# Kernel tuning notes

Hardware: AMD Instinct MI355X
Metric: run time of the kernel (lower is better)

## Reference

```python
import jax, jax.numpy as jnp
import numpy as np
from jax import lax

B, C, H, W = 32, 684, 28, 112   # batch, annotation channels, feature map HxW
Q, NP, N, K, PAD = 256, 512, 256, 11, 5  # f_channel, hidden_dim, decoder_dim, conv kernel, padding


def setup_inputs() -> dict:
    key = jax.random.key(0)
    ks = jax.random.split(key, 7)
    i = jax.random.normal(ks[0], (B, C, H, W), dtype=jnp.float32)
    hat_s_t = jax.random.normal(ks[1], (B, N), dtype=jnp.float32)
    alpha = jnp.zeros((B, 1, H, W), dtype=jnp.float32)  # coverage state (reset_alpha)
    conv_w = jax.random.normal(ks[2], (Q, 1, K, K), dtype=jnp.float32) * 0.02
    conv_b = jnp.zeros((Q,), dtype=jnp.float32)
    Wa = jax.random.normal(ks[3], (C, NP), dtype=jnp.float32) * (1.0 / np.sqrt(C))
    Wf = jax.random.normal(ks[4], (Q, NP), dtype=jnp.float32) * (1.0 / np.sqrt(Q))
    Ws = jax.random.normal(ks[5], (N, NP), dtype=jnp.float32) * (1.0 / np.sqrt(N))
    v = jax.random.normal(ks[6], (NP,), dtype=jnp.float32) * (1.0 / np.sqrt(NP))
    return {"i": i, "hat_s_t": hat_s_t, "alpha": alpha,
            "conv_w": conv_w, "conv_b": conv_b,
            "Wa": Wa, "Wf": Wf, "Ws": Ws, "v": v}


def reference(i, hat_s_t, alpha, conv_w, conv_b, Wa, Wf, Ws, v):
    b, c, h, w = i.shape
    L = h * w
    # coverage features: F = conv(alpha) -> [B, Q, H, W] -> [B, L, Q]
    F = lax.conv_general_dilated(
        alpha, conv_w, window_strides=(1, 1),
        padding=[(PAD, PAD), (PAD, PAD)],
        dimension_numbers=("NCHW", "OIHW", "NCHW"))
    F = F + conv_b[None, :, None, None]
    F = F.reshape(b, -1, L).transpose(0, 2, 1)          # [B, L, Q]
    A = i.reshape(b, c, L).transpose(0, 2, 1)           # [B, L, C]
    # additive attention energy e_t = v^T tanh(U_a A + U_f F + U_s s)
    pre = A @ Wa + F @ Wf + (hat_s_t @ Ws)[:, None, :]  # [B, L, NP]
    e = jnp.tanh(pre) @ v                               # [B, L]
    alpha_new = jax.nn.softmax(e, axis=1)               # softmax over L
    c_At = jnp.einsum("bl,blc->bc", alpha_new, A)       # context [B, C]
    return c_At
```

## Files before the change

kernel.cpp:

```cpp
#include <hip/hip_runtime.h>
#include <hip/hip_bf16.h>
#include <math.h>

#define B_   32
#define C_   684
#define H_   28
#define W_   112
#define L_   3136
#define Q_   256
#define NP_  512
#define N_   256
#define K_   11
#define KK_  121
#define KI_  684
#define KPATCH_ 805
#define KT_  832
#define KTILES_ 52
#define BM_  64
#define KC_  64
#define NCH_ 13

typedef short bf16x8  __attribute__((ext_vector_type(8)));
typedef float f32x16  __attribute__((ext_vector_type(16)));

#define MFMA32(a, b, c) __builtin_amdgcn_mfma_f32_32x32x16_bf16((a), (b), (c), 0, 0, 0)

__device__ __forceinline__ unsigned short f2bf(float x) {
  unsigned u = __float_as_uint(x);
  u += 0x7FFF + ((u >> 16) & 1);
  return (unsigned short)(u >> 16);
}
__device__ __forceinline__ short f2bf_fast(float x) {
  __hip_bfloat16 h = __float2bfloat16(x);
  return *reinterpret_cast<short*>(&h);
}

__global__ __launch_bounds__(256) void k_hsb(const float* __restrict__ s,
                                             const float* __restrict__ Ws,
                                             const float* __restrict__ conv_b,
                                             const float* __restrict__ Wf,
                                             float* __restrict__ hsb) {
  int b = blockIdx.x, t = threadIdx.x;
  int p0 = t, p1 = t + 256;
  float a0 = 0.f, a1 = 0.f;
  for (int n = 0; n < N_; n++) {
    float sv = s[b * N_ + n];
    a0 += sv * Ws[n * NP_ + p0];
    a1 += sv * Ws[n * NP_ + p1];
  }
  float b0 = 0.f, b1 = 0.f;
  for (int q = 0; q < Q_; q++) {
    float cb = conv_b[q];
    b0 += cb * Wf[q * NP_ + p0];
    b1 += cb * Wf[q * NP_ + p1];
  }
  hsb[b * NP_ + p0] = a0 + b0;
  hsb[b * NP_ + p1] = a1 + b1;
}

__global__ __launch_bounds__(256) void k_w2(const float* __restrict__ conv_w,
                                            const float* __restrict__ Wf,
                                            float* __restrict__ w2) {
  int kk = blockIdx.x, t = threadIdx.x;
  float a0 = 0.f, a1 = 0.f;
  for (int q = 0; q < Q_; q++) {
    float cw = conv_w[q * KK_ + kk];
    a0 += cw * Wf[q * NP_ + t];
    a1 += cw * Wf[q * NP_ + t + 256];
  }
  w2[kk * NP_ + t]       = a0;
  w2[kk * NP_ + t + 256] = a1;
}

__global__ __launch_bounds__(512) void k_wb(const float* __restrict__ Wa,
                                            const float* __restrict__ w2,
                                            unsigned short* __restrict__ Wbp) {
  const int k = blockIdx.x;
  const int p = threadIdx.x;
  float val = 0.f;
  if (k < KI_)          val = Wa[(size_t)k * NP_ + p];
  else if (k < KPATCH_) val = w2[(size_t)(k - KI_) * NP_ + p];
  const int ptile = p >> 5, ktile = k >> 4;
  const int lane = (p & 31) + (((k >> 3) & 1) << 5);
  const int kidx = k & 7;
  Wbp[((size_t)(ptile * KTILES_ + ktile)) * 512 + lane * 8 + kidx] = f2bf(val);
}

__global__ __launch_bounds__(512, 4) void k_energy(const float* __restrict__ i_,
                                                   const float* __restrict__ alpha,
                                                   const unsigned short* __restrict__ Wbp,
                                                   const float* __restrict__ hsb,
                                                   const float* __restrict__ v,
                                                   float* __restrict__ e_out) {
  __shared__ __attribute__((aligned(16))) unsigned char As[2][BM_ * 128];
  __shared__ float pe[8][BM_];

  const int tid = threadIdx.x, w = tid >> 6, lane = tid & 63;
  const int R0 = blockIdx.y * BM_;
  const int bb = R0 / L_;
  const int l0 = R0 - bb * L_;

  f32x16 acc[2];
#pragma unroll
  for (int mt = 0; mt < 2; mt++)
#pragma unroll
    for (int r = 0; r < 16; r++) acc[mt][r] = 0.f;

  const int sr = tid & 63;
  const int kq = (tid >> 6) * 8;
  const int sl = l0 + sr;
  const size_t ibase = (size_t)bb * ((size_t)C_ * L_) + sl;
  const int ly = sl / W_, lx = sl - ly * W_;

  float xs[8];
  auto stage_load = [&](int ch) {
    const int kb = ch * KC_ + kq;
    if (ch < 10) {
#pragma unroll
      for (int j = 0; j < 8; j++)
        xs[j] = i_[ibase + (size_t)(kb + j) * L_];
    } else {
#pragma unroll
      for (int j = 0; j < 8; j++) {
        int k = kb + j;
        float t = 0.f;
        if (k < KI_) {
          t = i_[ibase + (size_t)k * L_];
        } else if (k < KPATCH_) {
          int kkp = k - KI_;
          int ky = kkp / 11, kx = kkp - ky * 11;
          int yy = ly + ky - 5, xx = lx + kx - 5;
          if (yy >= 0 && yy < H_ && xx >= 0 && xx < W_)
            t = alpha[(size_t)bb * L_ + yy * W_ + xx];
        }
        xs[j] = t;
      }
    }
  };
  auto stage_write = [&](int buf) {
    bf16x8 hv;
#pragma unroll
    for (int j = 0; j < 8; j++) hv[j] = f2bf_fast(xs[j]);
    const int byte = sr * 128 + (((kq >> 3) ^ (sr & 7)) << 4);
    *(bf16x8*)(&As[buf][byte]) = hv;
  };

  stage_load(0);
  stage_write(0);
  __syncthreads();

  const int col = lane & 31, half = lane >> 5;
  const int abase0 = col * 128;
  const int abase1 = (col + 32) * 128;
  const int aswz = col & 7;
  const int pt = blockIdx.x * 8 + w;
  const unsigned short* wb = Wbp + ((size_t)pt * KTILES_) * 512 + lane * 8;

  bf16x8 ebh = *(const bf16x8*)(wb);
  bf16x8 obh = *(const bf16x8*)(wb + 512);

  int buf = 0;
  for (int ch = 0; ch < NCH_; ch++) {
    if (ch + 1 < NCH_) stage_load(ch + 1);

#pragma unroll
    for (int ks = 0; ks < 4; ks++) {
      const int g = ch * 4 + ks;
      const int soff = (((ks * 2 + half) ^ aswz) << 4);
      bf16x8 ah0 = *(const bf16x8*)(&As[buf][abase0 + soff]);
      bf16x8 ah1 = *(const bf16x8*)(&As[buf][abase1 + soff]);
      if ((ks & 1) == 0) {
        __builtin_amdgcn_s_setprio(1);
        acc[0] = MFMA32(ah0, ebh, acc[0]);
        acc[1] = MFMA32(ah1, ebh, acc[1]);
        __builtin_amdgcn_s_setprio(0);
        if (g + 2 < KTILES_)
          ebh = *(const bf16x8*)(wb + (size_t)(g + 2) * 512);
      } else {
        __builtin_amdgcn_s_setprio(1);
        acc[0] = MFMA32(ah0, obh, acc[0]);
        acc[1] = MFMA32(ah1, obh, acc[1]);
        __builtin_amdgcn_s_setprio(0);
        if (g + 2 < KTILES_)
          obh = *(const bf16x8*)(wb + (size_t)(g + 2) * 512);
      }
    }

    if (ch + 1 < NCH_) {
      stage_write(buf ^ 1);
      __syncthreads();
      buf ^= 1;
    }
  }

  const int pcol = blockIdx.x * 256 + w * 32 + col;
  const float h0 = hsb[bb * NP_ + pcol];
  const float v0 = v[pcol];
#pragma unroll
  for (int mt = 0; mt < 2; mt++) {
#pragma unroll
    for (int r = 0; r < 16; r++) {
      float val = v0 * tanhf(acc[mt][r] + h0);
      val += __shfl_xor(val, 16);
      val += __shfl_xor(val, 8);
      val += __shfl_xor(val, 4);
      val += __shfl_xor(val, 2);
      val += __shfl_xor(val, 1);
      if (col == 0) {
        int row = mt * 32 + (r & 3) + 8 * (r >> 2) + 4 * half;
        pe[w][row] = val;
      }
    }
  }
  __syncthreads();
  if (tid < BM_) {
    float s = 0.f;
#pragma unroll
    for (int ww = 0; ww < 8; ww++) s += pe[ww][tid];
    e_out[(size_t)blockIdx.x * (B_ * L_) + R0 + tid] = s;
  }
}

__global__ __launch_bounds__(256) void k_softmax(const float* __restrict__ e,
                                                 float* __restrict__ w) {
  __shared__ float sh[L_];
  __shared__ float red[4];
  const int b = blockIdx.x, tid = threadIdx.x;
  const int lane = tid & 63, wv = tid >> 6;

  float m = -1e30f;
  for (int idx = tid; idx < L_; idx += 256) {
    float t = e[(size_t)b * L_ + idx] + e[(size_t)B_ * L_ + (size_t)b * L_ + idx];
    sh[idx] = t;
    m = fmaxf(m, t);
  }
  m = fmaxf(m, __shfl_down(m, 32));
  m = fmaxf(m, __shfl_down(m, 16));
  m = fmaxf(m, __shfl_down(m, 8));
  m = fmaxf(m, __shfl_down(m, 4));
  m = fmaxf(m, __shfl_down(m, 2));
  m = fmaxf(m, __shfl_down(m, 1));
  if (lane == 0) red[wv] = m;
  __syncthreads();
  m = fmaxf(fmaxf(red[0], red[1]), fmaxf(red[2], red[3]));
  __syncthreads();

  float s = 0.f;
  for (int idx = tid; idx < L_; idx += 256) {
    float t = expf(sh[idx] - m);
    sh[idx] = t;
    s += t;
  }
  s += __shfl_down(s, 32);
  s += __shfl_down(s, 16);
  s += __shfl_down(s, 8);
  s += __shfl_down(s, 4);
  s += __shfl_down(s, 2);
  s += __shfl_down(s, 1);
  if (lane == 0) red[wv] = s;
  __syncthreads();
  float total = red[0] + red[1] + red[2] + red[3];
  float inv = 1.f / total;
  for (int idx = tid; idx < L_; idx += 256)
    w[(size_t)b * L_ + idx] = sh[idx] * inv;
}

__global__ __launch_bounds__(256) void k_context(const float* __restrict__ i_,
                                                 const float* __restrict__ w,
                                                 float* __restrict__ out) {
  __shared__ float red[4];
  const int b = blockIdx.y, c = blockIdx.x, tid = threadIdx.x;
  const int lane = tid & 63, wv = tid >> 6;
  const float4* row = (const float4*)(i_ + ((size_t)b * C_ + c) * L_);
  const float4* wr  = (const float4*)(w + (size_t)b * L_);
  float s = 0.f;
  for (int idx = tid; idx < L_ / 4; idx += 256) {
    float4 a = row[idx];
    float4 ww = wr[idx];
    s += a.x * ww.x + a.y * ww.y + a.z * ww.z + a.w * ww.w;
  }
  s += __shfl_down(s, 32);
  s += __shfl_down(s, 16);
  s += __shfl_down(s, 8);
  s += __shfl_down(s, 4);
  s += __shfl_down(s, 2);
  s += __shfl_down(s, 1);
  if (lane == 0) red[wv] = s;
  __syncthreads();
  if (tid == 0) out[(size_t)b * C_ + c] = red[0] + red[1] + red[2] + red[3];
}

extern "C" void kernel_launch(void* const* d_in, const int* in_sizes, int n_in,
                              void* d_out, int out_size, void* d_ws, size_t ws_size,
                              hipStream_t stream) {
  const float* i_      = (const float*)d_in[0];
  const float* hat_s_t = (const float*)d_in[1];
  const float* alpha   = (const float*)d_in[2];
  const float* conv_w  = (const float*)d_in[3];
  const float* conv_b  = (const float*)d_in[4];
  const float* Wa      = (const float*)d_in[5];
  const float* Wf      = (const float*)d_in[6];
  const float* Ws      = (const float*)d_in[7];
  const float* v       = (const float*)d_in[8];
  float* out = (float*)d_out;

  float* ws   = (float*)d_ws;
  float* hsb  = ws;
  float* w2   = hsb + B_ * NP_;
  float* e    = w2 + KK_ * NP_;
  float* anew = e + 2 * B_ * L_;
  unsigned short* Wbp = (unsigned short*)(anew + B_ * L_);

  k_hsb<<<dim3(B_), dim3(256), 0, stream>>>(hat_s_t, Ws, conv_b, Wf, hsb);
  k_w2<<<dim3(KK_), dim3(256), 0, stream>>>(conv_w, Wf, w2);
  k_wb<<<dim3(KT_), dim3(512), 0, stream>>>(Wa, w2, Wbp);
  k_energy<<<dim3(2, (B_ * L_) / BM_), dim3(512), 0, stream>>>(i_, alpha, Wbp, hsb, v, e);
  k_softmax<<<dim3(B_), dim3(256), 0, stream>>>(e, anew);
  k_context<<<dim3(C_, B_), dim3(256), 0, stream>>>(i_, anew, out);
}
```

Measured before the change: 315.4 us.

## Pre-pack activations to bf16 tiles and stream them into LDS with global_load_lds

Adds a prep kernel that reads the fp32 feature map and coverage im2col patches, transposes them through shared memory, and writes pre-swizzled bf16 tiles to workspace. The energy GEMM kernel then fills LDS directly with global_load_lds DMA instead of doing strided fp32 loads and conversion in registers. This is meant to remove the register staging and conversion from the MFMA loop and halve the bytes each energy block streams. The cost is an extra pass over the 280MB input plus a roughly 170MB bf16 intermediate written and read back. The old path is kept as a fallback when the workspace is too small.

```diff
diff --git a/kernel.cpp b/kernel.cpp
--- a/kernel.cpp
+++ b/kernel.cpp
@@ -19,6 +19,7 @@
 #define BM_  64
 #define KC_  64
 #define NCH_ 13
+#define NTILES_ 1568
 
 typedef short bf16x8  __attribute__((ext_vector_type(8)));
 typedef float f32x16  __attribute__((ext_vector_type(16)));
@@ -34,6 +35,9 @@
   __hip_bfloat16 h = __float2bfloat16(x);
   return *reinterpret_cast<short*>(&h);
 }
+
+typedef __attribute__((address_space(1))) const unsigned int* gas_ptr;
+typedef __attribute__((address_space(3))) unsigned int* las_ptr;
 
 __global__ __launch_bounds__(256) void k_hsb(const float* __restrict__ s,
                                              const float* __restrict__ Ws,
@@ -86,19 +90,65 @@
   Wbp[((size_t)(ptile * KTILES_ + ktile)) * 512 + lane * 8 + kidx] = f2bf(val);
 }
 
-__global__ __launch_bounds__(512, 4) void k_energy(const float* __restrict__ i_,
-                                                   const float* __restrict__ alpha,
-                                                   const unsigned short* __restrict__ Wbp,
-                                                   const float* __restrict__ hsb,
-                                                   const float* __restrict__ v,
-                                                   float* __restrict__ e_out) {
+__global__ __launch_bounds__(256) void k_prep(const float* __restrict__ i_,
+                                              const float* __restrict__ alpha,
+                                              unsigned short* __restrict__ A_pre) {
+  __shared__ float ftile[64][65];
+  const int tileR = blockIdx.x;
+  const int ch    = blockIdx.y;
+  const int tid = threadIdx.x;
+  const int R0 = tileR * BM_;
+  const int sb = R0 / L_;
+  const int l0 = R0 - sb * L_;
+  const int ll = tid & 63;
+  const int sl = l0 + ll;
+  const int ly = sl / W_, lx = sl - ly * W_;
+  const size_t ibase = (size_t)sb * ((size_t)C_ * L_) + sl;
+  const int k0 = ch * KC_;
+
+#pragma unroll
+  for (int kk = 0; kk < 16; kk++) {
+    const int kl = (tid >> 6) * 16 + kk;
+    const int k = k0 + kl;
+    float t = 0.f;
+    if (k < KI_) {
+      t = i_[ibase + (size_t)k * L_];
+    } else if (k < KPATCH_) {
+      int kkp = k - KI_;
+      int ky = kkp / 11, kx = kkp - ky * 11;
+      int yy = ly + ky - 5, xx = lx + kx - 5;
+      if (yy >= 0 && yy < H_ && xx >= 0 && xx < W_)
+        t = alpha[(size_t)sb * L_ + yy * W_ + xx];
+    }
+    ftile[kl][ll] = t;
+  }
+  __syncthreads();
+
+  unsigned short* outp = A_pre + ((size_t)tileR * NCH_ + ch) * 4096;
+#pragma unroll
+  for (int pass = 0; pass < 2; pass++) {
+    const int t = tid + pass * 256;
+    const int sr = t >> 3;
+    const int s  = t & 7;
+    const int kg = s ^ (sr & 7);
+    bf16x8 hv;
+#pragma unroll
+    for (int j = 0; j < 8; j++) hv[j] = f2bf_fast(ftile[kg * 8 + j][sr]);
+    *(bf16x8*)(outp + (size_t)t * 8) = hv;
+  }
+}
+
+__global__ __launch_bounds__(512, 4) void k_energy_lds(const unsigned short* __restrict__ A_pre,
+                                                       const unsigned short* __restrict__ Wbp,
+                                                       const float* __restrict__ hsb,
+                                                       const float* __restrict__ v,
+                                                       float* __restrict__ e_out) {
   __shared__ __attribute__((aligned(16))) unsigned char As[2][BM_ * 128];
   __shared__ float pe[8][BM_];
 
   const int tid = threadIdx.x, w = tid >> 6, lane = tid & 63;
   const int R0 = blockIdx.y * BM_;
   const int bb = R0 / L_;
-  const int l0 = R0 - bb * L_;
 
   f32x16 acc[2];
 #pragma unroll
@@ -106,47 +156,15 @@
 #pragma unroll
     for (int r = 0; r < 16; r++) acc[mt][r] = 0.f;
 
-  const int sr = tid & 63;
-  const int kq = (tid >> 6) * 8;
-  const int sl = l0 + sr;
-  const size_t ibase = (size_t)bb * ((size_t)C_ * L_) + sl;
-  const int ly = sl / W_, lx = sl - ly * W_;
-
-  float xs[8];
-  auto stage_load = [&](int ch) {
-    const int kb = ch * KC_ + kq;
-    if (ch < 10) {
-#pragma unroll
-      for (int j = 0; j < 8; j++)
-        xs[j] = i_[ibase + (size_t)(kb + j) * L_];
-    } else {
-#pragma unroll
-      for (int j = 0; j < 8; j++) {
-        int k = kb + j;
-        float t = 0.f;
-        if (k < KI_) {
-          t = i_[ibase + (size_t)k * L_];
-        } else if (k < KPATCH_) {
-          int kkp = k - KI_;
-          int ky = kkp / 11, kx = kkp - ky * 11;
-          int yy = ly + ky - 5, xx = lx + kx - 5;
-          if (yy >= 0 && yy < H_ && xx >= 0 && xx < W_)
-            t = alpha[(size_t)bb * L_ + yy * W_ + xx];
-        }
-        xs[j] = t;
-      }
-    }
+  const unsigned short* apre = A_pre + ((size_t)blockIdx.y * NCH_) * 4096;
+  auto stage = [&](int buf, int ch) {
+    const unsigned short* src = apre + (size_t)ch * 4096 + w * 512 + lane * 8;
+    __builtin_amdgcn_global_load_lds((gas_ptr)(const void*)src,
+                                     (las_ptr)(void*)(&As[buf][w * 1024]),
+                                     16, 0, 0);
   };
-  auto stage_write = [&](int buf) {
-    bf16x8 hv;
-#pragma unroll
-    for (int j = 0; j < 8; j++) hv[j] = f2bf_fast(xs[j]);
-    const int byte = sr * 128 + (((kq >> 3) ^ (sr & 7)) << 4);
-    *(bf16x8*)(&As[buf][byte]) = hv;
-  };
-
-  stage_load(0);
-  stage_write(0);
+
+  stage(0, 0);
   __syncthreads();
 
   const int col = lane & 31, half = lane >> 5;
@@ -161,7 +179,7 @@
 
   int buf = 0;
   for (int ch = 0; ch < NCH_; ch++) {
-    if (ch + 1 < NCH_) stage_load(ch + 1);
+    if (ch + 1 < NCH_) stage(buf ^ 1, ch + 1);
 
 #pragma unroll
     for (int ks = 0; ks < 4; ks++) {
@@ -187,6 +205,140 @@
     }
 
     if (ch + 1 < NCH_) {
+      __syncthreads();
+      buf ^= 1;
+    }
+  }
+
+  const int pcol = blockIdx.x * 256 + w * 32 + col;
+  const float h0 = hsb[bb * NP_ + pcol];
+  const float v0 = v[pcol];
+#pragma unroll
+  for (int mt = 0; mt < 2; mt++) {
+#pragma unroll
+    for (int r = 0; r < 16; r++) {
+      float val = v0 * tanhf(acc[mt][r] + h0);
+      val += __shfl_xor(val, 16);
+      val += __shfl_xor(val, 8);
+      val += __shfl_xor(val, 4);
+      val += __shfl_xor(val, 2);
+      val += __shfl_xor(val, 1);
+      if (col == 0) {
+        int row = mt * 32 + (r & 3) + 8 * (r >> 2) + 4 * half;
+        pe[w][row] = val;
+      }
+    }
+  }
+  __syncthreads();
+  if (tid < BM_) {
+    float s = 0.f;
+#pragma unroll
+    for (int ww = 0; ww < 8; ww++) s += pe[ww][tid];
+    e_out[(size_t)blockIdx.x * (B_ * L_) + R0 + tid] = s;
+  }
+}
+
+__global__ __launch_bounds__(512, 4) void k_energy_reg(const float* __restrict__ i_,
+                                                       const float* __restrict__ alpha,
+                                                       const unsigned short* __restrict__ Wbp,
+                                                       const float* __restrict__ hsb,
+                                                       const float* __restrict__ v,
+                                                       float* __restrict__ e_out) {
+  __shared__ __attribute__((aligned(16))) unsigned char As[2][BM_ * 128];
+  __shared__ float pe[8][BM_];
+
+  const int tid = threadIdx.x, w = tid >> 6, lane = tid & 63;
+  const int R0 = blockIdx.y * BM_;
+  const int bb = R0 / L_;
+  const int l0 = R0 - bb * L_;
+
+  f32x16 acc[2];
+#pragma unroll
+  for (int mt = 0; mt < 2; mt++)
+#pragma unroll
+    for (int r = 0; r < 16; r++) acc[mt][r] = 0.f;
+
+  const int sr = tid & 63;
+  const int kq = (tid >> 6) * 8;
+  const int sl = l0 + sr;
+  const size_t ibase = (size_t)bb * ((size_t)C_ * L_) + sl;
+  const int ly = sl / W_, lx = sl - ly * W_;
+
+  float xs[8];
+  auto stage_load = [&](int ch) {
+    const int kb = ch * KC_ + kq;
+    if (ch < 10) {
+#pragma unroll
+      for (int j = 0; j < 8; j++)
+        xs[j] = i_[ibase + (size_t)(kb + j) * L_];
+    } else {
+#pragma unroll
+      for (int j = 0; j < 8; j++) {
+        int k = kb + j;
+        float t = 0.f;
+        if (k < KI_) {
+          t = i_[ibase + (size_t)k * L_];
+        } else if (k < KPATCH_) {
+          int kkp = k - KI_;
+          int ky = kkp / 11, kx = kkp - ky * 11;
+          int yy = ly + ky - 5, xx = lx + kx - 5;
+          if (yy >= 0 && yy < H_ && xx >= 0 && xx < W_)
+            t = alpha[(size_t)bb * L_ + yy * W_ + xx];
+        }
+        xs[j] = t;
+      }
+    }
+  };
+  auto stage_write = [&](int buf) {
+    bf16x8 hv;
+#pragma unroll
+    for (int j = 0; j < 8; j++) hv[j] = f2bf_fast(xs[j]);
+    const int byte = sr * 128 + (((kq >> 3) ^ (sr & 7)) << 4);
+    *(bf16x8*)(&As[buf][byte]) = hv;
+  };
+
+  stage_load(0);
+  stage_write(0);
+  __syncthreads();
+
+  const int col = lane & 31, half = lane >> 5;
+  const int abase0 = col * 128;
+  const int abase1 = (col + 32) * 128;
+  const int aswz = col & 7;
+  const int pt = blockIdx.x * 8 + w;
+  const unsigned short* wb = Wbp + ((size_t)pt * KTILES_) * 512 + lane * 8;
+
+  bf16x8 ebh = *(const bf16x8*)(wb);
+  bf16x8 obh = *(const bf16x8*)(wb + 512);
+
+  int buf = 0;
+  for (int ch = 0; ch < NCH_; ch++) {
+    if (ch + 1 < NCH_) stage_load(ch + 1);
+
+#pragma unroll
+    for (int ks = 0; ks < 4; ks++) {
+      const int g = ch * 4 + ks;
+      const int soff = (((ks * 2 + half) ^ aswz) << 4);
+      bf16x8 ah0 = *(const bf16x8*)(&As[buf][abase0 + soff]);
+      bf16x8 ah1 = *(const bf16x8*)(&As[buf][abase1 + soff]);
+      if ((ks & 1) == 0) {
+        __builtin_amdgcn_s_setprio(1);
+        acc[0] = MFMA32(ah0, ebh, acc[0]);
+        acc[1] = MFMA32(ah1, ebh, acc[1]);
+        __builtin_amdgcn_s_setprio(0);
+        if (g + 2 < KTILES_)
+          ebh = *(const bf16x8*)(wb + (size_t)(g + 2) * 512);
+      } else {
+        __builtin_amdgcn_s_setprio(1);
+        acc[0] = MFMA32(ah0, obh, acc[0]);
+        acc[1] = MFMA32(ah1, obh, acc[1]);
+        __builtin_amdgcn_s_setprio(0);
+        if (g + 2 < KTILES_)
+          obh = *(const bf16x8*)(wb + (size_t)(g + 2) * 512);
+      }
+    }
+
+    if (ch + 1 < NCH_) {
       stage_write(buf ^ 1);
       __syncthreads();
       buf ^= 1;
@@ -310,11 +462,21 @@
   float* e    = w2 + KK_ * NP_;
   float* anew = e + 2 * B_ * L_;
   unsigned short* Wbp = (unsigned short*)(anew + B_ * L_);
+  size_t base_bytes = (size_t)((char*)(Wbp + (size_t)16 * KTILES_ * 512) - (char*)d_ws);
+  size_t apre_off   = (base_bytes + 255) & ~(size_t)255;
+  size_t apre_bytes = (size_t)NTILES_ * NCH_ * 8192;
+  unsigned short* A_pre = (unsigned short*)((char*)d_ws + apre_off);
+  const bool use_lds_path = (ws_size >= apre_off + apre_bytes);
 
   k_hsb<<<dim3(B_), dim3(256), 0, stream>>>(hat_s_t, Ws, conv_b, Wf, hsb);
   k_w2<<<dim3(KK_), dim3(256), 0, stream>>>(conv_w, Wf, w2);
   k_wb<<<dim3(KT_), dim3(512), 0, stream>>>(Wa, w2, Wbp);
-  k_energy<<<dim3(2, (B_ * L_) / BM_), dim3(512), 0, stream>>>(i_, alpha, Wbp, hsb, v, e);
+  if (use_lds_path) {
+    k_prep<<<dim3(NTILES_, NCH_), dim3(256), 0, stream>>>(i_, alpha, A_pre);
+    k_energy_lds<<<dim3(2, NTILES_), dim3(512), 0, stream>>>(A_pre, Wbp, hsb, v, e);
+  } else {
+    k_energy_reg<<<dim3(2, NTILES_), dim3(512), 0, stream>>>(i_, alpha, Wbp, hsb, v, e);
+  }
   k_softmax<<<dim3(B_), dim3(256), 0, stream>>>(e, anew);
   k_context<<<dim3(C_, B_), dim3(256), 0, stream>>>(i_, anew, out);
 }
```

New measurement: 376.3 us. 19.3% more time.

## Compute all 512 hidden columns per block to avoid reloading activations twice

Applied to the files above, without the earlier changes.

Each energy block now covers the full NP=512 output width, with each wave holding two 32-column tiles (a 2x2 MFMA accumulator tile), instead of splitting the hidden dimension across two blocks. The input activation tile is therefore read from global memory and converted to bf16 once rather than twice. The two partial energy buffers and their sum in the softmax kernel go away. In exchange each wave uses twice the accumulator registers and weight fragments, which may reduce occupancy under the 512x4 launch bounds, and the grid has half as many blocks.

```diff
diff --git a/kernel.cpp b/kernel.cpp
--- a/kernel.cpp
+++ b/kernel.cpp
@@ -96,15 +96,17 @@
   __shared__ float pe[8][BM_];
 
   const int tid = threadIdx.x, w = tid >> 6, lane = tid & 63;
-  const int R0 = blockIdx.y * BM_;
+  const int R0 = blockIdx.x * BM_;
   const int bb = R0 / L_;
   const int l0 = R0 - bb * L_;
 
-  f32x16 acc[2];
+  f32x16 acc[2][2];
 #pragma unroll
   for (int mt = 0; mt < 2; mt++)
 #pragma unroll
-    for (int r = 0; r < 16; r++) acc[mt][r] = 0.f;
+    for (int nt = 0; nt < 2; nt++)
+#pragma unroll
+      for (int r = 0; r < 16; r++) acc[mt][nt][r] = 0.f;
 
   const int sr = tid & 63;
   const int kq = (tid >> 6) * 8;
@@ -153,11 +155,13 @@
   const int abase0 = col * 128;
   const int abase1 = (col + 32) * 128;
   const int aswz = col & 7;
-  const int pt = blockIdx.x * 8 + w;
-  const unsigned short* wb = Wbp + ((size_t)pt * KTILES_) * 512 + lane * 8;
-
-  bf16x8 ebh = *(const bf16x8*)(wb);
-  bf16x8 obh = *(const bf16x8*)(wb + 512);
+  const unsigned short* wb0 = Wbp + ((size_t)(w * 2 + 0) * KTILES_) * 512 + lane * 8;
+  const unsigned short* wb1 = Wbp + ((size_t)(w * 2 + 1) * KTILES_) * 512 + lane * 8;
+
+  bf16x8 eb0 = *(const bf16x8*)(wb0);
+  bf16x8 eb1 = *(const bf16x8*)(wb1);
+  bf16x8 ob0 = *(const bf16x8*)(wb0 + 512);
+  bf16x8 ob1 = *(const bf16x8*)(wb1 + 512);
 
   int buf = 0;
   for (int ch = 0; ch < NCH_; ch++) {
@@ -171,18 +175,28 @@
       bf16x8 ah1 = *(const bf16x8*)(&As[buf][abase1 + soff]);
       if ((ks & 1) == 0) {
         __builtin_amdgcn_s_setprio(1);
-        acc[0] = MFMA32(ah0, ebh, acc[0]);
-        acc[1] = MFMA32(ah1, ebh, acc[1]);
+        acc[0][0] = MFMA32(ah0, eb0, acc[0][0]);
+        acc[0][1] = MFMA32(ah0, eb1, acc[0][1]);
+        acc[1][0] = MFMA32(ah1, eb0, acc[1][0]);
+        acc[1][1] = MFMA32(ah1, eb1, acc[1][1]);
         __builtin_amdgcn_s_setprio(0);
-        if (g + 2 < KTILES_)
-          ebh = *(const bf16x8*)(wb + (size_t)(g + 2) * 512);
+        if (g + 2 < KTILES_) {
+          const size_t o = (size_t)(g + 2) * 512;
+          eb0 = *(const bf16x8*)(wb0 + o);
+          eb1 = *(const bf16x8*)(wb1 + o);
+        }
       } else {
         __builtin_amdgcn_s_setprio(1);
-        acc[0] = MFMA32(ah0, obh, acc[0]);
-        acc[1] = MFMA32(ah1, obh, acc[1]);
+        acc[0][0] = MFMA32(ah0, ob0, acc[0][0]);
+        acc[0][1] = MFMA32(ah0, ob1, acc[0][1]);
+        acc[1][0] = MFMA32(ah1, ob0, acc[1][0]);
+        acc[1][1] = MFMA32(ah1, ob1, acc[1][1]);
         __builtin_amdgcn_s_setprio(0);
-        if (g + 2 < KTILES_)
-          obh = *(const bf16x8*)(wb + (size_t)(g + 2) * 512);
+        if (g + 2 < KTILES_) {
+          const size_t o = (size_t)(g + 2) * 512;
+          ob0 = *(const bf16x8*)(wb0 + o);
+          ob1 = *(const bf16x8*)(wb1 + o);
+        }
       }
     }
 
@@ -193,14 +207,14 @@
     }
   }
 
-  const int pcol = blockIdx.x * 256 + w * 32 + col;
-  const float h0 = hsb[bb * NP_ + pcol];
-  const float v0 = v[pcol];
+  const int p0 = w * 64 + col, p1 = p0 + 32;
+  const float h0 = hsb[bb * NP_ + p0], h1 = hsb[bb * NP_ + p1];
+  const float v0 = v[p0], v1 = v[p1];
 #pragma unroll
   for (int mt = 0; mt < 2; mt++) {
 #pragma unroll
     for (int r = 0; r < 16; r++) {
-      float val = v0 * tanhf(acc[mt][r] + h0);
+      float val = v0 * tanhf(acc[mt][0][r] + h0) + v1 * tanhf(acc[mt][1][r] + h1);
       val += __shfl_xor(val, 16);
       val += __shfl_xor(val, 8);
       val += __shfl_xor(val, 4);
@@ -217,7 +231,7 @@
     float s = 0.f;
 #pragma unroll
     for (int ww = 0; ww < 8; ww++) s += pe[ww][tid];
-    e_out[(size_t)blockIdx.x * (B_ * L_) + R0 + tid] = s;
+    e_out[(size_t)(R0 + tid)] = s;
   }
 }
 
@@ -230,7 +244,7 @@
 
   float m = -1e30f;
   for (int idx = tid; idx < L_; idx += 256) {
-    float t = e[(size_t)b * L_ + idx] + e[(size_t)B_ * L_ + (size_t)b * L_ + idx];
+    float t = e[(size_t)b * L_ + idx];
     sh[idx] = t;
     m = fmaxf(m, t);
   }
@@ -308,13 +322,13 @@
   float* hsb  = ws;
   float* w2   = hsb + B_ * NP_;
   float* e    = w2 + KK_ * NP_;
-  float* anew = e + 2 * B_ * L_;
+  float* anew = e + B_ * L_;
   unsigned short* Wbp = (unsigned short*)(anew + B_ * L_);
 
   k_hsb<<<dim3(B_), dim3(256), 0, stream>>>(hat_s_t, Ws, conv_b, Wf, hsb);
   k_w2<<<dim3(KK_), dim3(256), 0, stream>>>(conv_w, Wf, w2);
   k_wb<<<dim3(KT_), dim3(512), 0, stream>>>(Wa, w2, Wbp);
-  k_energy<<<dim3(2, (B_ * L_) / BM_), dim3(512), 0, stream>>>(i_, alpha, Wbp, hsb, v, e);
+  k_energy<<<dim3((B_ * L_) / BM_), dim3(512), 0, stream>>>(i_, alpha, Wbp, hsb, v, e);
   k_softmax<<<dim3(B_), dim3(256), 0, stream>>>(e, anew);
   k_context<<<dim3(C_, B_), dim3(256), 0, stream>>>(i_, anew, out);
 }
```

Result: faster. 271.2 us (-14.0%).
